# Performance work log

Hardware: AMD Instinct MI355X
Metric: run time of the kernel (lower is better)

Reference implementation:

```python
import jax, jax.numpy as jnp
import numpy as np

D_MODEL = 1024
N_HEAD = 16
D_K = D_MODEL // N_HEAD
B, S = 2, 2048


def setup_inputs() -> dict:
    key = jax.random.key(0)
    ks = jax.random.split(key, 12)
    sc = 1.0 / np.sqrt(D_MODEL)
    return {
        "q": jax.random.normal(ks[0], (B, S, D_MODEL), jnp.float32),
        "k": jax.random.normal(ks[1], (B, S, D_MODEL), jnp.float32),
        "v": jax.random.normal(ks[2], (B, S, D_MODEL), jnp.float32),
        "mask": jax.random.randint(ks[3], (B, S, S), 0, 2, jnp.int32),
        # learned params (torch Linear convention: y = x @ W + b with W pre-transposed)
        "wq": jax.random.normal(ks[4], (D_MODEL, D_MODEL), jnp.float32) * sc,
        "bq": jax.random.normal(ks[5], (D_MODEL,), jnp.float32) * sc,
        "wk": jax.random.normal(ks[6], (D_MODEL, D_MODEL), jnp.float32) * sc,  # no bias
        "wv": jax.random.normal(ks[7], (D_MODEL, D_MODEL), jnp.float32) * sc,
        "bv": jax.random.normal(ks[8], (D_MODEL,), jnp.float32) * sc,
        "wf": jax.random.normal(ks[9], (D_MODEL, D_MODEL), jnp.float32) * sc,
        "bf": jax.random.normal(ks[10], (D_MODEL,), jnp.float32) * sc,
    }


def reference(q, k, v, mask, wq, bq, wk, wv, bv, wf, bf):
    bs = q.shape[0]
    temperature = jnp.asarray(D_K ** 0.5, q.dtype)
    # projections -> [b, h, s, d_k]
    qh = (q @ wq + bq).reshape(bs, -1, N_HEAD, D_K).transpose(0, 2, 1, 3)
    kh = (k @ wk).reshape(bs, -1, N_HEAD, D_K).transpose(0, 2, 1, 3)
    vh = (v @ wv + bv).reshape(bs, -1, N_HEAD, D_K).transpose(0, 2, 1, 3)
    # scores [b, h, sq, sk]
    attn = jnp.einsum("bhqd,bhkd->bhqk", qh, kh) / temperature
    m0 = (mask[:, None, :, :] == 0)  # mask==0 -> masked out, broadcast over heads
    attn = jnp.where(m0, -jnp.inf, attn)
    attn = jax.nn.softmax(attn, axis=-1)
    attn = jnp.where(m0, 0.0, attn)
    out = jnp.einsum("bhqk,bhkd->bhqd", attn, vh)
    out = out.transpose(0, 2, 1, 3).reshape(bs, -1, D_MODEL)
    return out @ wf + bf  # dropout is identity in eval mode
```

## Files before the change

### kernel.cpp

```cpp
#include <hip/hip_runtime.h>

#define D_MODEL 1024
#define NHEAD   16
#define DK      64
#define BATCH   2
#define SEQ     2048

typedef __attribute__((ext_vector_type(8))) short bf16x8;
typedef __attribute__((ext_vector_type(4))) float f32x4;

#define QSCALE 0.18033688011f

__device__ __forceinline__ unsigned short f2b(float x) {
  unsigned u = __builtin_bit_cast(unsigned, x);
  u = (u + 0x7fffu + ((u >> 16) & 1u)) >> 16;
  return (unsigned short)u;
}
__device__ __forceinline__ unsigned short f2b_rhu(float x) {
  return (unsigned short)((__builtin_bit_cast(unsigned, x) + 0x8000u) >> 16);
}
__device__ __forceinline__ int pk2(float a, float b) {
  unsigned ua = __builtin_bit_cast(unsigned, a) + 0x8000u;
  unsigned ub = __builtin_bit_cast(unsigned, b) + 0x8000u;
  return (int)__builtin_amdgcn_perm(ub, ua, 0x07060302u);
}

typedef const __attribute__((address_space(1))) void* gas_p;
typedef __attribute__((address_space(3))) void* las_p;
__device__ __forceinline__ void gll16(const void* g, void* l) {
  __builtin_amdgcn_global_load_lds((gas_p)g, (las_p)l, 16, 0, 0);
}

__global__ __launch_bounds__(256) void cast3_kernel(
    const float* __restrict__ q, const float* __restrict__ k, const float* __restrict__ v,
    unsigned short* __restrict__ qb, unsigned short* __restrict__ kb,
    unsigned short* __restrict__ vb) {
  const float* src = blockIdx.y == 0 ? q : (blockIdx.y == 1 ? k : v);
  unsigned short* dst = blockIdx.y == 0 ? qb : (blockIdx.y == 1 ? kb : vb);
  size_t i = ((size_t)blockIdx.x * 256 + threadIdx.x) * 8;
  float4 x0 = *(const float4*)&src[i];
  float4 x1 = *(const float4*)&src[i + 4];
  int4 w;
  w.x = pk2(x0.x, x0.y); w.y = pk2(x0.z, x0.w);
  w.z = pk2(x1.x, x1.y); w.w = pk2(x1.z, x1.w);
  *(int4*)&dst[i] = w;
}

__global__ __launch_bounds__(256) void wtrans_kernel(
    const float* __restrict__ wq, const float* __restrict__ wk,
    const float* __restrict__ wv, const float* __restrict__ wf,
    unsigned short* __restrict__ wqt, unsigned short* __restrict__ wkt,
    unsigned short* __restrict__ wvt, unsigned short* __restrict__ wft) {
  __shared__ float tile[64][65];
  const float* w; unsigned short* wt;
  switch (blockIdx.z) {
    case 0: w = wq; wt = wqt; break;
    case 1: w = wk; wt = wkt; break;
    case 2: w = wv; wt = wvt; break;
    default: w = wf; wt = wft; break;
  }
  int r0 = blockIdx.y * 64, c0 = blockIdx.x * 64;
  int t = threadIdx.x;
  for (int i = 0; i < 16; ++i) {
    int idx = t + i * 256; int r = idx >> 6, c = idx & 63;
    tile[r][c] = w[(size_t)(r0 + r) * D_MODEL + c0 + c];
  }
  __syncthreads();
  for (int i = 0; i < 16; ++i) {
    int idx = t + i * 256; int r = idx >> 6, c = idx & 63;
    wt[(size_t)(c0 + r) * D_MODEL + r0 + c] = f2b(tile[c][r]);
  }
}

__global__ __launch_bounds__(256) void maskpack_kernel(
    const int* __restrict__ mask, unsigned long long* __restrict__ mbits) {
  size_t gw = ((size_t)blockIdx.x * 256 + threadIdx.x) >> 6;
  int lane = threadIdx.x & 63;
  int val = mask[gw * 64 + lane];
  unsigned long long bits = __ballot(val != 0);
  if (lane == 0) mbits[gw] = bits;
}

__global__ __launch_bounds__(256) void gemm_qkv_kernel(
    const unsigned short* __restrict__ qb, const unsigned short* __restrict__ kb,
    const unsigned short* __restrict__ vb,
    const unsigned short* __restrict__ wqt, const unsigned short* __restrict__ wkt,
    const unsigned short* __restrict__ wvt,
    const float* __restrict__ bq, const float* __restrict__ bv,
    unsigned short* __restrict__ qh, unsigned short* __restrict__ kh,
    unsigned short* __restrict__ vt) {
  __shared__ unsigned short SB[16640];
  unsigned short* As = SB;
  unsigned short* Bs = SB + 8192;
  int bid = blockIdx.x;
  int xcd = bid & 7, slot = bid >> 3;
  int mi = slot & 3, zn = slot >> 2;
  int z = zn >> 3;
  int n0 = (zn & 7) * 128;
  int m0 = (mi * 8 + xcd) * 128;
  const unsigned short* A; const unsigned short* Bt;
  switch (z) {
    case 0:  A = qb; Bt = wqt; break;
    case 1:  A = kb; Bt = wkt; break;
    default: A = vb; Bt = wvt; break;
  }
  int t = threadIdx.x, lane = t & 63, wave = t >> 6;
  int l16 = lane & 15, quad = lane >> 4;
  int wm = (wave & 1) * 64, wn = (wave >> 1) * 64;
  f32x4 zero = {0.f, 0.f, 0.f, 0.f};
  f32x4 acc[4][4];
  for (int mt = 0; mt < 4; ++mt) for (int nt = 0; nt < 4; ++nt) acc[mt][nt] = zero;

  int drow = lane >> 2, dcol = (lane & 3) * 8;
  const unsigned short* asrc = A  + (size_t)(m0 + wave * 32 + drow) * D_MODEL + dcol;
  const unsigned short* bsrc = Bt + (size_t)(n0 + wave * 32 + drow) * D_MODEL + dcol;
  unsigned short* adst = As + wave * 32 * 32 + lane * 8;
  unsigned short* bdst = Bs + wave * 32 * 32 + lane * 8;

  for (int k0 = 0; k0 < D_MODEL; k0 += 64) {
    __syncthreads();
#pragma unroll
    for (int g = 0; g < 2; ++g)
#pragma unroll
      for (int hf = 0; hf < 2; ++hf) {
        gll16(asrc + (size_t)(g * 16) * D_MODEL + k0 + hf * 32, adst + hf * 4096 + g * 512);
        gll16(bsrc + (size_t)(g * 16) * D_MODEL + k0 + hf * 32, bdst + hf * 4096 + g * 512);
      }
    __syncthreads();
#pragma unroll
    for (int half = 0; half < 2; ++half) {
      bf16x8 a[4], b[4];
      for (int mt = 0; mt < 4; ++mt)
        a[mt] = *(const bf16x8*)&As[half * 4096 + (wm + mt * 16 + l16) * 32 + quad * 8];
      for (int nt = 0; nt < 4; ++nt)
        b[nt] = *(const bf16x8*)&Bs[half * 4096 + (wn + nt * 16 + l16) * 32 + quad * 8];
      for (int mt = 0; mt < 4; ++mt)
        for (int nt = 0; nt < 4; ++nt)
          acc[mt][nt] = __builtin_amdgcn_mfma_f32_16x16x32_bf16(a[mt], b[nt], acc[mt][nt], 0, 0, 0);
    }
  }

  if (z == 2) {
    __syncthreads();
#pragma unroll
    for (int nt = 0; nt < 4; ++nt) {
      int col = wn + nt * 16 + l16;
      float bb = bv[n0 + col];
      for (int mt = 0; mt < 4; ++mt)
        for (int r = 0; r < 4; ++r)
          SB[col * 130 + wm + mt * 16 + quad * 4 + r] = f2b_rhu(acc[mt][nt][r] + bb);
    }
    __syncthreads();
    int c = t >> 1, hf = t & 1;
    int colg = n0 + c, hh = colg >> 6, dd = colg & 63;
    int b_ = m0 >> 11, sbase = m0 & (SEQ - 1);
    unsigned short* dst = vt + (((size_t)(b_ * NHEAD + hh)) * DK + dd) * SEQ + sbase + hf * 64;
#pragma unroll
    for (int j = 0; j < 8; ++j)
      *(int4*)(dst + j * 8) = *(const int4*)&SB[c * 130 + hf * 64 + j * 8];
  } else if (z == 0) {
    for (int nt = 0; nt < 4; ++nt) {
      int col = n0 + wn + nt * 16 + l16;
      float bb = bq[col];
      int h = col >> 6, d = col & 63;
      for (int mt = 0; mt < 4; ++mt)
        for (int r = 0; r < 4; ++r) {
          int row = m0 + wm + mt * 16 + quad * 4 + r;
          int b_ = row >> 11, s = row & (SEQ - 1);
          qh[(((size_t)(b_ * NHEAD + h) * SEQ) + s) * DK + d] =
              f2b_rhu((acc[mt][nt][r] + bb) * QSCALE);
        }
    }
  } else {
    for (int nt = 0; nt < 4; ++nt) {
      int col = n0 + wn + nt * 16 + l16;
      int h = col >> 6, d = col & 63;
      for (int mt = 0; mt < 4; ++mt)
        for (int r = 0; r < 4; ++r) {
          int row = m0 + wm + mt * 16 + quad * 4 + r;
          int b_ = row >> 11, s = row & (SEQ - 1);
          kh[(((size_t)(b_ * NHEAD + h) * SEQ) + s) * DK + d] = f2b_rhu(acc[mt][nt][r]);
        }
    }
  }
}

__global__ __launch_bounds__(256) void gemm_out_kernel(
    const unsigned short* __restrict__ A, const unsigned short* __restrict__ Bt,
    const float* __restrict__ bias, float* __restrict__ out) {
  __shared__ unsigned short As[64 * 64], Bs[64 * 64];
  int bid = blockIdx.x;
  int xcd = bid & 7, slot = bid >> 3;
  int mi = slot & 7, n0 = (slot >> 3) * 64;
  int m0 = (mi * 8 + xcd) * 64;
  int t = threadIdx.x, lane = t & 63, wave = t >> 6;
  int l16 = lane & 15, quad = lane >> 4;
  int wm = (wave & 1) * 32, wn = (wave >> 1) * 32;
  f32x4 zero = {0.f, 0.f, 0.f, 0.f};
  f32x4 acc[2][2];
  for (int mt = 0; mt < 2; ++mt) for (int nt = 0; nt < 2; ++nt) acc[mt][nt] = zero;

  int drow = lane >> 2, dcol = (lane & 3) * 8;
  const unsigned short* asrc = A  + (size_t)(m0 + wave * 16 + drow) * D_MODEL + dcol;
  const unsigned short* bsrc = Bt + (size_t)(n0 + wave * 16 + drow) * D_MODEL + dcol;
  unsigned short* adst = As + wave * 512 + lane * 8;
  unsigned short* bdst = Bs + wave * 512 + lane * 8;

  for (int k0 = 0; k0 < D_MODEL; k0 += 64) {
    __syncthreads();
#pragma unroll
    for (int hf = 0; hf < 2; ++hf) {
      gll16(asrc + k0 + hf * 32, adst + hf * 2048);
      gll16(bsrc + k0 + hf * 32, bdst + hf * 2048);
    }
    __syncthreads();
#pragma unroll
    for (int half = 0; half < 2; ++half) {
      bf16x8 a[2], b[2];
      for (int mt = 0; mt < 2; ++mt)
        a[mt] = *(const bf16x8*)&As[half * 2048 + (wm + mt * 16 + l16) * 32 + quad * 8];
      for (int nt = 0; nt < 2; ++nt)
        b[nt] = *(const bf16x8*)&Bs[half * 2048 + (wn + nt * 16 + l16) * 32 + quad * 8];
      for (int mt = 0; mt < 2; ++mt)
        for (int nt = 0; nt < 2; ++nt)
          acc[mt][nt] = __builtin_amdgcn_mfma_f32_16x16x32_bf16(a[mt], b[nt], acc[mt][nt], 0, 0, 0);
    }
  }
  for (int nt = 0; nt < 2; ++nt) {
    int col = n0 + wn + nt * 16 + l16;
    float bb = bias[col];
    for (int mt = 0; mt < 2; ++mt)
      for (int r = 0; r < 4; ++r) {
        int row = m0 + wm + mt * 16 + quad * 4 + r;
        out[(size_t)row * D_MODEL + col] = acc[mt][nt][r] + bb;
      }
  }
}

__global__ __launch_bounds__(256) void attn_kernel(
    const unsigned short* __restrict__ qh, const unsigned short* __restrict__ kh,
    const unsigned short* __restrict__ vt, const unsigned long long* __restrict__ mbits,
    unsigned short* __restrict__ attb) {
  __shared__ unsigned short Qs[64 * 72];
  __shared__ unsigned short Ks[64 * 64], Vs[64 * 64];
  int bid = blockIdx.x;
  int xcd = bid & 7, slot = bid >> 3;
  int bh_ = 4 * xcd + (slot >> 5);
  int qt = slot & 31;
  int b = bh_ >> 4, h = bh_ & 15;
  int t = threadIdx.x, lane = t & 63, wave = t >> 6;
  int l16 = lane & 15, quad = lane >> 4;
  size_t bh = (size_t)b * NHEAD + h;

  int sr = t >> 2, sc = (t & 3) * 8;
  const unsigned short* Qg = qh + (bh * SEQ + (size_t)qt * 64) * DK;
  *(int4*)&Qs[sr * 72 + sc]      = *(const int4*)&Qg[sr * DK + sc];
  *(int4*)&Qs[sr * 72 + sc + 32] = *(const int4*)&Qg[sr * DK + sc + 32];
  __syncthreads();
  bf16x8 qf[2];
  qf[0] = *(const bf16x8*)&Qs[(wave * 16 + l16) * 72 + quad * 8];
  qf[1] = *(const bf16x8*)&Qs[(wave * 16 + l16) * 72 + 32 + quad * 8];
  unsigned short* Pw = &Qs[wave * 1088];

  const unsigned short* Kg = kh + bh * SEQ * DK;
  const unsigned short* Vg = vt + bh * DK * SEQ;
  const unsigned long long* mrow = mbits + (size_t)b * SEQ * (SEQ / 64);
  int qrow0 = qt * 64 + wave * 16 + quad * 4;

  int drow = lane >> 2, dcol = (lane & 3) * 8;
  unsigned short* kdst = Ks + wave * 512 + lane * 8;
  unsigned short* vdst = Vs + wave * 512 + lane * 8;

  bf16x8 ones;
#pragma unroll
  for (int i = 0; i < 8; ++i) ones[i] = (short)0x3F80;

  f32x4 zero = {0.f, 0.f, 0.f, 0.f};
  f32x4 accO[4], accRS = zero;
  for (int nt = 0; nt < 4; ++nt) accO[nt] = zero;

  for (int tk = 0; tk < SEQ / 64; ++tk) {
    __syncthreads();
    {
      const unsigned short* Kt = Kg + ((size_t)tk * 64 + wave * 16 + drow) * DK + dcol;
      const unsigned short* Vt_ = Vg + (size_t)(wave * 16 + drow) * SEQ + tk * 64 + dcol;
#pragma unroll
      for (int hf = 0; hf < 2; ++hf) {
        gll16(Kt + hf * 32, kdst + hf * 2048);
        gll16(Vt_ + hf * 32, vdst + hf * 2048);
      }
    }
    __syncthreads();

    unsigned long long mw[4];
#pragma unroll
    for (int r = 0; r < 4; ++r)
      mw[r] = mrow[(size_t)(qrow0 + r) * (SEQ / 64) + tk] >> l16;

    f32x4 accS[4];
    for (int nt = 0; nt < 4; ++nt) accS[nt] = zero;
#pragma unroll
    for (int step = 0; step < 2; ++step)
      for (int nt = 0; nt < 4; ++nt) {
        bf16x8 bk = *(const bf16x8*)&Ks[step * 2048 + (nt * 16 + l16) * 32 + quad * 8];
        accS[nt] = __builtin_amdgcn_mfma_f32_16x16x32_bf16(qf[step], bk, accS[nt], 0, 0, 0);
      }

#pragma unroll
    for (int r = 0; r < 4; ++r) {
      unsigned lo = (unsigned)mw[r], hi = (unsigned)(mw[r] >> 32);
#pragma unroll
      for (int nt = 0; nt < 4; ++nt) {
        unsigned halfw = (nt < 2) ? lo : hi;
        const int sh = 31 - ((nt & 1) * 16);
        float pv = __builtin_amdgcn_exp2f(accS[nt][r]);
        unsigned u = (__builtin_bit_cast(unsigned, pv) + 0x8000u) >> 16;
        int mskv = ((int)(halfw << sh)) >> 31;
        Pw[(quad * 4 + r) * 68 + nt * 16 + l16] = (unsigned short)(u & (unsigned)mskv);
      }
    }

#pragma unroll
    for (int step = 0; step < 2; ++step) {
      short4 plo = *(const short4*)&Pw[l16 * 68 + step * 32 + quad * 8];
      short4 phi = *(const short4*)&Pw[l16 * 68 + step * 32 + quad * 8 + 4];
      bf16x8 ap = {plo.x, plo.y, plo.z, plo.w, phi.x, phi.y, phi.z, phi.w};
      accRS = __builtin_amdgcn_mfma_f32_16x16x32_bf16(ap, ones, accRS, 0, 0, 0);
      for (int nt = 0; nt < 4; ++nt) {
        bf16x8 bv_ = *(const bf16x8*)&Vs[step * 2048 + (nt * 16 + l16) * 32 + quad * 8];
        accO[nt] = __builtin_amdgcn_mfma_f32_16x16x32_bf16(ap, bv_, accO[nt], 0, 0, 0);
      }
    }
  }

  for (int r = 0; r < 4; ++r) {
    float sden = accRS[r];
    float inv = sden > 0.f ? 1.f / sden : 0.f;
    int row = qt * 64 + wave * 16 + quad * 4 + r;
    size_t ob = ((size_t)b * SEQ + row) * D_MODEL + (size_t)h * DK;
    for (int nt = 0; nt < 4; ++nt)
      attb[ob + nt * 16 + l16] = f2b_rhu(accO[nt][r] * inv);
  }
}

extern "C" void kernel_launch(void* const* d_in, const int* in_sizes, int n_in,
                              void* d_out, int out_size, void* d_ws, size_t ws_size,
                              hipStream_t stream) {
  (void)in_sizes; (void)n_in; (void)out_size; (void)ws_size;
  const float* q    = (const float*)d_in[0];
  const float* k    = (const float*)d_in[1];
  const float* v    = (const float*)d_in[2];
  const int*   mask = (const int*)d_in[3];
  const float* wq   = (const float*)d_in[4];
  const float* bq   = (const float*)d_in[5];
  const float* wk   = (const float*)d_in[6];
  const float* wv   = (const float*)d_in[7];
  const float* bv   = (const float*)d_in[8];
  const float* wf   = (const float*)d_in[9];
  const float* bf   = (const float*)d_in[10];

  char* ws = (char*)d_ws;
  unsigned short* wft  = (unsigned short*)(ws + 0);
  unsigned short* wqt  = (unsigned short*)(ws + 2097152);
  unsigned short* wkt  = (unsigned short*)(ws + 4194304);
  unsigned short* wvt  = (unsigned short*)(ws + 6291456);
  unsigned short* attb = (unsigned short*)(ws + 2097152);
  unsigned short* qhp  = (unsigned short*)(ws + 10485760);
  unsigned short* khp  = (unsigned short*)(ws + 18874368);
  unsigned short* vtp  = (unsigned short*)(ws + 27262976);
  unsigned long long* mbits = (unsigned long long*)(ws + 35651584);
  unsigned short* vb   = (unsigned short*)(ws + 36700160);
  unsigned short* qb   = (unsigned short*)d_out;
  unsigned short* kb   = (unsigned short*)d_out + 4194304;

  hipLaunchKernelGGL(cast3_kernel, dim3(2048, 3), dim3(256), 0, stream, q, k, v, qb, kb, vb);
  hipLaunchKernelGGL(wtrans_kernel, dim3(16, 16, 4), dim3(256), 0, stream,
                     wq, wk, wv, wf, wqt, wkt, wvt, wft);
  hipLaunchKernelGGL(maskpack_kernel, dim3(32768), dim3(256), 0, stream, mask, mbits);
  hipLaunchKernelGGL(gemm_qkv_kernel, dim3(768), dim3(256), 0, stream,
                     qb, kb, vb, wqt, wkt, wvt, bq, bv, qhp, khp, vtp);
  hipLaunchKernelGGL(attn_kernel, dim3(1024), dim3(256), 0, stream,
                     qhp, khp, vtp, mbits, attb);
  hipLaunchKernelGGL(gemm_out_kernel, dim3(1024), dim3(256), 0, stream,
                     attb, wft, bf, (float*)d_out);
}
```

Before: 300.6 us.

## Double-buffer LDS tiles in QKV, output GEMM and attention loops

Adds ping-pong shared-memory buffers so the next K-slice (or next K tile in attention) is fetched with async global-to-LDS loads while the current one is consumed by MFMA. This leaves one barrier per iteration in the GEMMs. The QKV GEMM now steps 32 along K per iteration instead of 64. Attention loads Q fragments straight from global memory, moves P into its own LDS region, and issues V loads early, with a barrier placed before the P write. LDS use per block goes up, which may lower occupancy, and correctness depends on the async loads completing before each barrier.

```diff
diff --git a/kernel.cpp b/kernel.cpp
--- a/kernel.cpp
+++ b/kernel.cpp
@@ -90,8 +90,6 @@
     unsigned short* __restrict__ qh, unsigned short* __restrict__ kh,
     unsigned short* __restrict__ vt) {
   __shared__ unsigned short SB[16640];
-  unsigned short* As = SB;
-  unsigned short* Bs = SB + 8192;
   int bid = blockIdx.x;
   int xcd = bid & 7, slot = bid >> 3;
   int mi = slot & 3, zn = slot >> 2;
@@ -114,30 +112,32 @@
   int drow = lane >> 2, dcol = (lane & 3) * 8;
   const unsigned short* asrc = A  + (size_t)(m0 + wave * 32 + drow) * D_MODEL + dcol;
   const unsigned short* bsrc = Bt + (size_t)(n0 + wave * 32 + drow) * D_MODEL + dcol;
-  unsigned short* adst = As + wave * 32 * 32 + lane * 8;
-  unsigned short* bdst = Bs + wave * 32 * 32 + lane * 8;
-
-  for (int k0 = 0; k0 < D_MODEL; k0 += 64) {
-    __syncthreads();
-#pragma unroll
-    for (int g = 0; g < 2; ++g)
-#pragma unroll
-      for (int hf = 0; hf < 2; ++hf) {
-        gll16(asrc + (size_t)(g * 16) * D_MODEL + k0 + hf * 32, adst + hf * 4096 + g * 512);
-        gll16(bsrc + (size_t)(g * 16) * D_MODEL + k0 + hf * 32, bdst + hf * 4096 + g * 512);
-      }
-    __syncthreads();
-#pragma unroll
-    for (int half = 0; half < 2; ++half) {
-      bf16x8 a[4], b[4];
-      for (int mt = 0; mt < 4; ++mt)
-        a[mt] = *(const bf16x8*)&As[half * 4096 + (wm + mt * 16 + l16) * 32 + quad * 8];
+  int dst = wave * 1024 + lane * 8;
+
+#pragma unroll
+  for (int g = 0; g < 2; ++g) {
+    gll16(asrc + (size_t)(g * 16) * D_MODEL, &SB[dst + g * 512]);
+    gll16(bsrc + (size_t)(g * 16) * D_MODEL, &SB[4096 + dst + g * 512]);
+  }
+  for (int it = 0; it < 32; ++it) {
+    __syncthreads();
+    if (it + 1 < 32) {
+      int nb = ((it + 1) & 1) * 8192, kn = (it + 1) * 32;
+#pragma unroll
+      for (int g = 0; g < 2; ++g) {
+        gll16(asrc + (size_t)(g * 16) * D_MODEL + kn, &SB[nb + dst + g * 512]);
+        gll16(bsrc + (size_t)(g * 16) * D_MODEL + kn, &SB[nb + 4096 + dst + g * 512]);
+      }
+    }
+    int cb = (it & 1) * 8192;
+    bf16x8 a[4], b[4];
+    for (int mt = 0; mt < 4; ++mt)
+      a[mt] = *(const bf16x8*)&SB[cb + (wm + mt * 16 + l16) * 32 + quad * 8];
+    for (int nt = 0; nt < 4; ++nt)
+      b[nt] = *(const bf16x8*)&SB[cb + 4096 + (wn + nt * 16 + l16) * 32 + quad * 8];
+    for (int mt = 0; mt < 4; ++mt)
       for (int nt = 0; nt < 4; ++nt)
-        b[nt] = *(const bf16x8*)&Bs[half * 4096 + (wn + nt * 16 + l16) * 32 + quad * 8];
-      for (int mt = 0; mt < 4; ++mt)
-        for (int nt = 0; nt < 4; ++nt)
-          acc[mt][nt] = __builtin_amdgcn_mfma_f32_16x16x32_bf16(a[mt], b[nt], acc[mt][nt], 0, 0, 0);
-    }
+        acc[mt][nt] = __builtin_amdgcn_mfma_f32_16x16x32_bf16(a[mt], b[nt], acc[mt][nt], 0, 0, 0);
   }
 
   if (z == 2) {
@@ -154,10 +154,10 @@
     int c = t >> 1, hf = t & 1;
     int colg = n0 + c, hh = colg >> 6, dd = colg & 63;
     int b_ = m0 >> 11, sbase = m0 & (SEQ - 1);
-    unsigned short* dst = vt + (((size_t)(b_ * NHEAD + hh)) * DK + dd) * SEQ + sbase + hf * 64;
+    unsigned short* dstp = vt + (((size_t)(b_ * NHEAD + hh)) * DK + dd) * SEQ + sbase + hf * 64;
 #pragma unroll
     for (int j = 0; j < 8; ++j)
-      *(int4*)(dst + j * 8) = *(const int4*)&SB[c * 130 + hf * 64 + j * 8];
+      *(int4*)(dstp + j * 8) = *(const int4*)&SB[c * 130 + hf * 64 + j * 8];
   } else if (z == 0) {
     for (int nt = 0; nt < 4; ++nt) {
       int col = n0 + wn + nt * 16 + l16;
@@ -188,7 +188,7 @@
 __global__ __launch_bounds__(256) void gemm_out_kernel(
     const unsigned short* __restrict__ A, const unsigned short* __restrict__ Bt,
     const float* __restrict__ bias, float* __restrict__ out) {
-  __shared__ unsigned short As[64 * 64], Bs[64 * 64];
+  __shared__ unsigned short As[8192], Bs[8192];
   int bid = blockIdx.x;
   int xcd = bid & 7, slot = bid >> 3;
   int mi = slot & 7, n0 = (slot >> 3) * 64;
@@ -203,24 +203,31 @@
   int drow = lane >> 2, dcol = (lane & 3) * 8;
   const unsigned short* asrc = A  + (size_t)(m0 + wave * 16 + drow) * D_MODEL + dcol;
   const unsigned short* bsrc = Bt + (size_t)(n0 + wave * 16 + drow) * D_MODEL + dcol;
-  unsigned short* adst = As + wave * 512 + lane * 8;
-  unsigned short* bdst = Bs + wave * 512 + lane * 8;
-
-  for (int k0 = 0; k0 < D_MODEL; k0 += 64) {
-    __syncthreads();
-#pragma unroll
-    for (int hf = 0; hf < 2; ++hf) {
-      gll16(asrc + k0 + hf * 32, adst + hf * 2048);
-      gll16(bsrc + k0 + hf * 32, bdst + hf * 2048);
-    }
-    __syncthreads();
+  int dst = wave * 512 + lane * 8;
+
+#pragma unroll
+  for (int hf = 0; hf < 2; ++hf) {
+    gll16(asrc + hf * 32, &As[dst + hf * 2048]);
+    gll16(bsrc + hf * 32, &Bs[dst + hf * 2048]);
+  }
+  for (int it = 0; it < 16; ++it) {
+    __syncthreads();
+    if (it + 1 < 16) {
+      int nb = ((it + 1) & 1) * 4096, kn = (it + 1) * 64;
+#pragma unroll
+      for (int hf = 0; hf < 2; ++hf) {
+        gll16(asrc + kn + hf * 32, &As[nb + dst + hf * 2048]);
+        gll16(bsrc + kn + hf * 32, &Bs[nb + dst + hf * 2048]);
+      }
+    }
+    int cb = (it & 1) * 4096;
 #pragma unroll
     for (int half = 0; half < 2; ++half) {
       bf16x8 a[2], b[2];
       for (int mt = 0; mt < 2; ++mt)
-        a[mt] = *(const bf16x8*)&As[half * 2048 + (wm + mt * 16 + l16) * 32 + quad * 8];
+        a[mt] = *(const bf16x8*)&As[cb + half * 2048 + (wm + mt * 16 + l16) * 32 + quad * 8];
       for (int nt = 0; nt < 2; ++nt)
-        b[nt] = *(const bf16x8*)&Bs[half * 2048 + (wn + nt * 16 + l16) * 32 + quad * 8];
+        b[nt] = *(const bf16x8*)&Bs[cb + half * 2048 + (wn + nt * 16 + l16) * 32 + quad * 8];
       for (int mt = 0; mt < 2; ++mt)
         for (int nt = 0; nt < 2; ++nt)
           acc[mt][nt] = __builtin_amdgcn_mfma_f32_16x16x32_bf16(a[mt], b[nt], acc[mt][nt], 0, 0, 0);
@@ -241,8 +248,9 @@
     const unsigned short* __restrict__ qh, const unsigned short* __restrict__ kh,
     const unsigned short* __restrict__ vt, const unsigned long long* __restrict__ mbits,
     unsigned short* __restrict__ attb) {
-  __shared__ unsigned short Qs[64 * 72];
-  __shared__ unsigned short Ks[64 * 64], Vs[64 * 64];
+  __shared__ unsigned short Ks[8192];
+  __shared__ unsigned short Vs[4096];
+  __shared__ unsigned short Ps[4352];
   int bid = blockIdx.x;
   int xcd = bid & 7, slot = bid >> 3;
   int bh_ = 4 * xcd + (slot >> 5);
@@ -252,15 +260,11 @@
   int l16 = lane & 15, quad = lane >> 4;
   size_t bh = (size_t)b * NHEAD + h;
 
-  int sr = t >> 2, sc = (t & 3) * 8;
-  const unsigned short* Qg = qh + (bh * SEQ + (size_t)qt * 64) * DK;
-  *(int4*)&Qs[sr * 72 + sc]      = *(const int4*)&Qg[sr * DK + sc];
-  *(int4*)&Qs[sr * 72 + sc + 32] = *(const int4*)&Qg[sr * DK + sc + 32];
-  __syncthreads();
+  const unsigned short* Qg = qh + (bh * SEQ + (size_t)(qt * 64 + wave * 16 + l16)) * DK;
   bf16x8 qf[2];
-  qf[0] = *(const bf16x8*)&Qs[(wave * 16 + l16) * 72 + quad * 8];
-  qf[1] = *(const bf16x8*)&Qs[(wave * 16 + l16) * 72 + 32 + quad * 8];
-  unsigned short* Pw = &Qs[wave * 1088];
+  qf[0] = *(const bf16x8*)&Qg[quad * 8];
+  qf[1] = *(const bf16x8*)&Qg[32 + quad * 8];
+  unsigned short* Pw = &Ps[wave * 1088];
 
   const unsigned short* Kg = kh + bh * SEQ * DK;
   const unsigned short* Vg = vt + bh * DK * SEQ;
@@ -268,8 +272,8 @@
   int qrow0 = qt * 64 + wave * 16 + quad * 4;
 
   int drow = lane >> 2, dcol = (lane & 3) * 8;
-  unsigned short* kdst = Ks + wave * 512 + lane * 8;
-  unsigned short* vdst = Vs + wave * 512 + lane * 8;
+  int dst = wave * 512 + lane * 8;
+  const unsigned short* Vrow = Vg + (size_t)(wave * 16 + drow) * SEQ + dcol;
 
   bf16x8 ones;
 #pragma unroll
@@ -279,33 +283,39 @@
   f32x4 accO[4], accRS = zero;
   for (int nt = 0; nt < 4; ++nt) accO[nt] = zero;
 
+  {
+    const unsigned short* Kt = Kg + (size_t)(wave * 16 + drow) * DK + dcol;
+#pragma unroll
+    for (int hf = 0; hf < 2; ++hf) gll16(Kt + hf * 32, &Ks[dst + hf * 2048]);
+  }
+
   for (int tk = 0; tk < SEQ / 64; ++tk) {
     __syncthreads();
-    {
-      const unsigned short* Kt = Kg + ((size_t)tk * 64 + wave * 16 + drow) * DK + dcol;
-      const unsigned short* Vt_ = Vg + (size_t)(wave * 16 + drow) * SEQ + tk * 64 + dcol;
-#pragma unroll
-      for (int hf = 0; hf < 2; ++hf) {
-        gll16(Kt + hf * 32, kdst + hf * 2048);
-        gll16(Vt_ + hf * 32, vdst + hf * 2048);
-      }
-    }
-    __syncthreads();
+    if (tk + 1 < SEQ / 64) {
+      int nb = ((tk + 1) & 1) * 4096;
+      const unsigned short* Kt = Kg + (size_t)((tk + 1) * 64 + wave * 16 + drow) * DK + dcol;
+#pragma unroll
+      for (int hf = 0; hf < 2; ++hf) gll16(Kt + hf * 32, &Ks[nb + dst + hf * 2048]);
+    }
+#pragma unroll
+    for (int hf = 0; hf < 2; ++hf) gll16(Vrow + tk * 64 + hf * 32, &Vs[dst + hf * 2048]);
 
     unsigned long long mw[4];
 #pragma unroll
     for (int r = 0; r < 4; ++r)
       mw[r] = mrow[(size_t)(qrow0 + r) * (SEQ / 64) + tk] >> l16;
 
+    int cb = (tk & 1) * 4096;
     f32x4 accS[4];
     for (int nt = 0; nt < 4; ++nt) accS[nt] = zero;
 #pragma unroll
     for (int step = 0; step < 2; ++step)
       for (int nt = 0; nt < 4; ++nt) {
-        bf16x8 bk = *(const bf16x8*)&Ks[step * 2048 + (nt * 16 + l16) * 32 + quad * 8];
+        bf16x8 bk = *(const bf16x8*)&Ks[cb + step * 2048 + (nt * 16 + l16) * 32 + quad * 8];
         accS[nt] = __builtin_amdgcn_mfma_f32_16x16x32_bf16(qf[step], bk, accS[nt], 0, 0, 0);
       }
 
+    unsigned short pb[4][4];
 #pragma unroll
     for (int r = 0; r < 4; ++r) {
       unsigned lo = (unsigned)mw[r], hi = (unsigned)(mw[r] >> 32);
@@ -316,9 +326,16 @@
         float pv = __builtin_amdgcn_exp2f(accS[nt][r]);
         unsigned u = (__builtin_bit_cast(unsigned, pv) + 0x8000u) >> 16;
         int mskv = ((int)(halfw << sh)) >> 31;
-        Pw[(quad * 4 + r) * 68 + nt * 16 + l16] = (unsigned short)(u & (unsigned)mskv);
-      }
-    }
+        pb[r][nt] = (unsigned short)(u & (unsigned)mskv);
+      }
+    }
+
+    __syncthreads();
+#pragma unroll
+    for (int r = 0; r < 4; ++r)
+#pragma unroll
+      for (int nt = 0; nt < 4; ++nt)
+        Pw[(quad * 4 + r) * 68 + nt * 16 + l16] = pb[r][nt];
 
 #pragma unroll
     for (int step = 0; step < 2; ++step) {
```

New measurement: 295.2 us. About the same (-1.8%).
